# Kernel optimization log

Measured on AMD Instinct MI355X. Metric: run time of the kernel, lower is better.

Reference implementation:

```python
import jax, jax.numpy as jnp
import numpy as np

N_EMB = 1024
NUM_HEADS = 16
HEAD_DIM = N_EMB // NUM_HEADS
B, T = 4, 2048


def setup_inputs() -> dict:
    key = jax.random.key(0)
    k1, k2, k3, k4, k5 = jax.random.split(key, 5)
    s = 0.02
    return {
        "x": jax.random.normal(k1, (B, T, N_EMB), dtype=jnp.float32),
        "w_qkv": jax.random.normal(k2, (N_EMB, 3 * N_EMB), dtype=jnp.float32) * s,
        "b_qkv": jnp.zeros((3 * N_EMB,), dtype=jnp.float32),
        "w_proj": jax.random.normal(k3, (N_EMB, N_EMB), dtype=jnp.float32) * s,
        "b_proj": jnp.zeros((N_EMB,), dtype=jnp.float32),
    }


def reference(x, w_qkv, b_qkv, w_proj, b_proj):
    Bx, Tx, C = x.shape
    qkv = x @ w_qkv + b_qkv  # [B,T,3C]
    q, k, v = jnp.split(qkv, 3, axis=-1)
    # [B,H,T,D]
    def heads(t):
        return t.reshape(Bx, Tx, NUM_HEADS, HEAD_DIM).transpose(0, 2, 1, 3)
    q, k, v = heads(q), heads(k), heads(v)
    scale = 1.0 / np.sqrt(HEAD_DIM).astype(np.float32)
    att = jnp.einsum('bhqd,bhkd->bhqk', q, k) * scale
    causal = jnp.tril(jnp.ones((Tx, Tx), dtype=bool))
    att = jnp.where(causal[None, None], att, -jnp.inf)
    att = jax.nn.softmax(att, axis=-1)
    # dropout omitted (eval mode / deterministic reference)
    y = jnp.einsum('bhqk,bhkd->bhqd', att, v)
    y = y.transpose(0, 2, 1, 3).reshape(Bx, Tx, C)
    return y @ w_proj + b_proj
```

## Files before the change

### kernel.cpp

```cpp
#include <hip/hip_runtime.h>
#include <hip/hip_bf16.h>

typedef __attribute__((ext_vector_type(8))) short short8;
typedef __attribute__((ext_vector_type(4))) float f32x4;

static __device__ __forceinline__ unsigned short f2bf(float f) {
    unsigned int u = __builtin_bit_cast(unsigned int, f);
    u += 0x7fff + ((u >> 16) & 1);
    return (unsigned short)(u >> 16);
}

static __device__ __forceinline__ float bf2f(unsigned short u) {
    return __builtin_bit_cast(float, (unsigned int)u << 16);
}

static __device__ __forceinline__ void gl_lds16(const unsigned short* g, unsigned short* l) {
    __builtin_amdgcn_global_load_lds(
        (const __attribute__((address_space(1))) unsigned int*)g,
        (__attribute__((address_space(3))) unsigned int*)l, 16, 0, 0);
}

__global__ __launch_bounds__(256) void k_f32_to_bf16(
    const float* __restrict__ in, unsigned short* __restrict__ out, long n)
{
    long i = ((long)blockIdx.x * 256 + threadIdx.x) * 8;
    if (i >= n) return;
    const f32x4 a = *reinterpret_cast<const f32x4*>(in + i);
    const f32x4 b = *reinterpret_cast<const f32x4*>(in + i + 4);
    union { unsigned short u[8]; uint4 v; } o;
    o.u[0] = f2bf(a[0]); o.u[1] = f2bf(a[1]); o.u[2] = f2bf(a[2]); o.u[3] = f2bf(a[3]);
    o.u[4] = f2bf(b[0]); o.u[5] = f2bf(b[1]); o.u[6] = f2bf(b[2]); o.u[7] = f2bf(b[3]);
    *reinterpret_cast<uint4*>(out + i) = o.v;
}

__global__ __launch_bounds__(256) void k_transpose_w(
    const float* __restrict__ w, unsigned short* __restrict__ wt, int K, int N)
{
    __shared__ unsigned short tile[64][72];
    const int k0 = blockIdx.x * 64, n0 = blockIdx.y * 64;
    const int tid = threadIdx.x;
#pragma unroll
    for (int it = 0; it < 4; ++it) {
        int idx = it * 256 + tid;
        int kl = idx >> 4;
        int nl = (idx & 15) * 4;
        f32x4 v = *reinterpret_cast<const f32x4*>(w + (long)(k0 + kl) * N + n0 + nl);
        tile[kl][nl + 0] = f2bf(v[0]);
        tile[kl][nl + 1] = f2bf(v[1]);
        tile[kl][nl + 2] = f2bf(v[2]);
        tile[kl][nl + 3] = f2bf(v[3]);
    }
    __syncthreads();
#pragma unroll
    for (int it = 0; it < 2; ++it) {
        int idx = it * 256 + tid;
        int nl = idx >> 3;
        int c  = (idx & 7) * 8;
        union { unsigned short u[8]; uint4 v; } o;
#pragma unroll
        for (int j = 0; j < 8; ++j) o.u[j] = tile[c + j][nl];
        *reinterpret_cast<uint4*>(wt + (long)(n0 + nl) * K + k0 + c) = o.v;
    }
}

template <int OUTF32>
__global__ __launch_bounds__(256) void k_gemm_bt(
    const unsigned short* __restrict__ A,
    const unsigned short* __restrict__ Bt,
    const float* __restrict__ bias,
    void* __restrict__ Cv, int M, int N, int K)
{
    __shared__ unsigned short As[128][72];
    __shared__ unsigned short Bs[128][72];
    const int tid = threadIdx.x;
    const int m0 = blockIdx.x * 128;
    const int n0 = blockIdx.y * 128;
    const int w = tid >> 6, lane = tid & 63;
    const int wr = (w >> 1) * 64, wc = (w & 1) * 64;
    const int l4 = lane >> 4, l15 = lane & 15;

    f32x4 acc[4][4] = {};
    const int nk = K / 64;
    for (int kt = 0; kt < nk; ++kt) {
        const int k0 = kt * 64;
        __syncthreads();
#pragma unroll
        for (int it = 0; it < 4; ++it) {
            int idx = it * 256 + tid;
            int r = idx >> 3, c = (idx & 7) * 8;
            *reinterpret_cast<uint4*>(&As[r][c]) =
                *reinterpret_cast<const uint4*>(A + (long)(m0 + r) * K + k0 + c);
            *reinterpret_cast<uint4*>(&Bs[r][c]) =
                *reinterpret_cast<const uint4*>(Bt + (long)(n0 + r) * K + k0 + c);
        }
        __syncthreads();
#pragma unroll
        for (int kk = 0; kk < 2; ++kk) {
            short8 af[4], bf[4];
#pragma unroll
            for (int m = 0; m < 4; ++m)
                af[m] = *reinterpret_cast<const short8*>(&As[wr + m * 16 + l15][kk * 32 + l4 * 8]);
#pragma unroll
            for (int n = 0; n < 4; ++n)
                bf[n] = *reinterpret_cast<const short8*>(&Bs[wc + n * 16 + l15][kk * 32 + l4 * 8]);
#pragma unroll
            for (int m = 0; m < 4; ++m)
#pragma unroll
                for (int n = 0; n < 4; ++n)
                    acc[m][n] = __builtin_amdgcn_mfma_f32_16x16x32_bf16(af[m], bf[n], acc[m][n], 0, 0, 0);
        }
    }
#pragma unroll
    for (int n = 0; n < 4; ++n) {
        const int col = n0 + wc + n * 16 + l15;
        const float bv = bias[col];
#pragma unroll
        for (int m = 0; m < 4; ++m) {
            const int row = m0 + wr + m * 16 + l4 * 4;
#pragma unroll
            for (int i = 0; i < 4; ++i) {
                float v = acc[m][n][i] + bv;
                if (OUTF32)
                    reinterpret_cast<float*>(Cv)[(long)(row + i) * N + col] = v;
                else
                    reinterpret_cast<unsigned short*>(Cv)[(long)(row + i) * N + col] = f2bf(v);
            }
        }
    }
}

__global__ __launch_bounds__(256) void k_transpose_v(
    const unsigned short* __restrict__ qkv, unsigned short* __restrict__ vt, int T)
{
    __shared__ unsigned short tile[64][72];
    const int t0 = blockIdx.x * 64, bh = blockIdx.y;
    const int b = bh >> 4, h = bh & 15;
    const int tid = threadIdx.x;
#pragma unroll
    for (int it = 0; it < 2; ++it) {
        int idx = it * 256 + tid;
        int r = idx >> 3, c = (idx & 7) * 8;
        *reinterpret_cast<uint4*>(&tile[r][c]) =
            *reinterpret_cast<const uint4*>(qkv + (long)(b * T + t0 + r) * 3072 + 2048 + h * 64 + c);
    }
    __syncthreads();
#pragma unroll
    for (int it = 0; it < 2; ++it) {
        int idx = it * 256 + tid;
        int d = idx >> 3, c = (idx & 7) * 8;
        union { unsigned short u[8]; uint4 v; } o;
#pragma unroll
        for (int j = 0; j < 8; ++j) o.u[j] = tile[c + j][d];
        *reinterpret_cast<uint4*>(vt + ((long)bh * 64 + d) * T + t0 + c) = o.v;
    }
}

__global__ __launch_bounds__(256, 3) void k_attn(
    const unsigned short* __restrict__ qkv,
    const unsigned short* __restrict__ vt,
    unsigned short* __restrict__ y, int T)
{
    __shared__ __align__(16) unsigned short Kb[2][64][64];
    __shared__ __align__(16) unsigned short Vb[2][64][64];
    __shared__ unsigned short Ps[4][16][64];
    const int nQT = T >> 6;

    int n = blockIdx.x + gridDim.x * blockIdx.y;
    n = (n & 7) * ((gridDim.x * gridDim.y) >> 3) + (n >> 3);
    const int qa = n & 15;
    const int qb = nQT - 1 - qa;
    const int bh = n >> 4;
    const int b = bh >> 4, h = bh & 15;
    const int tid = threadIdx.x, w = tid >> 6, lane = tid & 63;
    const int l4 = lane >> 4, l15 = lane & 15;

    const float SC = 0.125f * 1.44269504f;

    const unsigned short* qpA = qkv + (long)(b * T + qa * 64 + w * 16 + l15) * 3072 + h * 64;
    const unsigned short* qpB = qkv + (long)(b * T + qb * 64 + w * 16 + l15) * 3072 + h * 64;
    short8 qfA[2], qfB[2];
    qfA[0] = *reinterpret_cast<const short8*>(qpA + l4 * 8);
    qfA[1] = *reinterpret_cast<const short8*>(qpA + 32 + l4 * 8);
    qfB[0] = *reinterpret_cast<const short8*>(qpB + l4 * 8);
    qfB[1] = *reinterpret_cast<const short8*>(qpB + 32 + l4 * 8);
#pragma unroll
    for (int kk = 0; kk < 2; ++kk)
#pragma unroll
        for (int j = 0; j < 8; ++j) {
            qfA[kk][j] = (short)f2bf(bf2f((unsigned short)qfA[kk][j]) * SC);
            qfB[kk][j] = (short)f2bf(bf2f((unsigned short)qfB[kk][j]) * SC);
        }

    short8 onesf;
#pragma unroll
    for (int j = 0; j < 8; ++j) onesf[j] = (short)0x3F80;

    const int lrow  = lane >> 3;
    const int lslot = (lane & 7) ^ lrow;
    const unsigned short* kg = qkv + (long)b * T * 3072 + 1024 + h * 64 + lslot * 8;
    const unsigned short* vg = vt + (long)bh * 64 * T + lslot * 8;

    auto stage = [&](int buf, int kt) {
#pragma unroll
        for (int i = 0; i < 2; ++i) {
            const int rb = (w * 2 + i) * 8;
            gl_lds16(kg + (long)(kt * 64 + rb + lrow) * 3072, &Kb[buf][rb][0]);
            gl_lds16(vg + (long)(rb + lrow) * T + kt * 64,    &Vb[buf][rb][0]);
        }
    };

    f32x4 oA[4] = {}, oB[4] = {};
    f32x4 lsA = {}, lsB = {};
    const int qrow = w * 16 + l4 * 4;
    int cur = 0;

    auto do_tile = [&](const short8 (&qf)[2], f32x4 (&o)[4], f32x4 &ls,
                       bool diag) {
        f32x4 s[4] = {};
        __builtin_amdgcn_s_setprio(1);
#pragma unroll
        for (int kk = 0; kk < 2; ++kk)
#pragma unroll
            for (int c = 0; c < 4; ++c) {
                const int r = c * 16 + l15;
                short8 kf = *reinterpret_cast<const short8*>(
                    &Kb[cur][r][(((kk * 4 + l4) ^ (r & 7)) * 8)]);
                s[c] = __builtin_amdgcn_mfma_f32_16x16x32_bf16(qf[kk], kf, s[c], 0, 0, 0);
            }
        __builtin_amdgcn_s_setprio(0);
#pragma unroll
        for (int c = 0; c < 4; ++c)
#pragma unroll
            for (int i = 0; i < 4; ++i) {
                float p = exp2f(s[c][i]);
                if (diag && (c * 16 + l15 > qrow + i)) p = 0.f;
                const int pr = l4 * 4 + i;
                Ps[w][pr][(c * 16 + l15) ^ ((pr & 7) << 3)] =
                    (unsigned short)(__builtin_bit_cast(unsigned int, p) >> 16);
            }
        __builtin_amdgcn_s_setprio(1);
#pragma unroll
        for (int kk = 0; kk < 2; ++kk) {
            short8 pf = *reinterpret_cast<const short8*>(
                &Ps[w][l15][(((kk * 4 + l4) ^ (l15 & 7)) * 8)]);
            ls = __builtin_amdgcn_mfma_f32_16x16x32_bf16(pf, onesf, ls, 0, 0, 0);
#pragma unroll
            for (int nn = 0; nn < 4; ++nn) {
                const int r = nn * 16 + l15;
                short8 vf = *reinterpret_cast<const short8*>(
                    &Vb[cur][r][(((kk * 4 + l4) ^ (r & 7)) * 8)]);
                o[nn] = __builtin_amdgcn_mfma_f32_16x16x32_bf16(pf, vf, o[nn], 0, 0, 0);
            }
        }
        __builtin_amdgcn_s_setprio(0);
    };

    stage(0, 0);
    __syncthreads();
    for (int kt = 0; kt <= qb; ++kt) {
        if (kt < qb) stage(cur ^ 1, kt + 1);
        do_tile(qfB, oB, lsB, kt == qb);
        if (kt <= qa) do_tile(qfA, oA, lsA, kt == qa);
        __syncthreads();
        cur ^= 1;
    }

#pragma unroll
    for (int i = 0; i < 4; ++i) {
        float invA = 1.f / lsA[i];
        float invB = 1.f / lsB[i];
        int qArow = qa * 64 + w * 16 + l4 * 4 + i;
        int qBrow = qb * 64 + w * 16 + l4 * 4 + i;
        unsigned short* ypA = y + (long)(b * T + qArow) * 1024 + h * 64;
        unsigned short* ypB = y + (long)(b * T + qBrow) * 1024 + h * 64;
#pragma unroll
        for (int nn = 0; nn < 4; ++nn) {
            ypA[nn * 16 + l15] = f2bf(oA[nn][i] * invA);
            ypB[nn * 16 + l15] = f2bf(oB[nn][i] * invB);
        }
    }
}

extern "C" void kernel_launch(void* const* d_in, const int* in_sizes, int n_in,
                              void* d_out, int out_size, void* d_ws, size_t ws_size,
                              hipStream_t stream) {
    const float* x      = (const float*)d_in[0];
    const float* w_qkv  = (const float*)d_in[1];
    const float* b_qkv  = (const float*)d_in[2];
    const float* w_proj = (const float*)d_in[3];
    const float* b_proj = (const float*)d_in[4];
    float* out = (float*)d_out;

    const int B = 4, T = 2048, C = 1024, H = 16;
    const long M = (long)B * T;

    char* ws = (char*)d_ws;
    unsigned short* xb  = (unsigned short*)ws; ws += M * C * 2;
    unsigned short* wqt = (unsigned short*)ws; ws += (long)3 * C * C * 2;
    unsigned short* wpt = (unsigned short*)ws; ws += (long)C * C * 2;
    unsigned short* qkv = (unsigned short*)ws; ws += M * 3 * C * 2;
    unsigned short* vt  = (unsigned short*)ws; ws += M * C * 2;
    unsigned short* y   = (unsigned short*)ws; ws += M * C * 2;

    k_f32_to_bf16<<<(int)((M * C / 8 + 255) / 256), 256, 0, stream>>>(x, xb, M * C);
    {
        dim3 g(C / 64, 3 * C / 64);
        k_transpose_w<<<g, 256, 0, stream>>>(w_qkv, wqt, C, 3 * C);
    }
    {
        dim3 g(C / 64, C / 64);
        k_transpose_w<<<g, 256, 0, stream>>>(w_proj, wpt, C, C);
    }
    {
        dim3 g(M / 128, 3 * C / 128);
        k_gemm_bt<0><<<g, 256, 0, stream>>>(xb, wqt, b_qkv, qkv, (int)M, 3 * C, C);
    }
    {
        dim3 g(T / 64, B * H);
        k_transpose_v<<<g, 256, 0, stream>>>(qkv, vt, T);
    }
    {
        dim3 g(T / 128, B * H);
        k_attn<<<g, 256, 0, stream>>>(qkv, vt, y, T);
    }
    {
        dim3 g(M / 128, C / 128);
        k_gemm_bt<1><<<g, 256, 0, stream>>>(y, wpt, b_proj, out, (int)M, C, C);
    }
}
```

Before: 190.2 us.

## Switch attention to 32x32x16 MFMA with transposed scores and register P exchange

Rewrites the attention inner loop to compute S^T with 32x32x16 bf16 MFMAs, so that each wave handles its 16 rows of both paired query tiles (A and B) together in one 32-column block. The probabilities are packed to bf16 and swapped between half-waves with shuffles instead of a round trip through the LDS Ps buffer, and the output is written as packed 8-byte stores. Dropping the Ps shared array and raising the launch-bounds occupancy target from 3 to 4 aims at more waves per CU. In exchange, the A-tile lanes do masked but still-executed work on key tiles beyond their causal limit, and register pressure is higher under the tighter launch bound.

```diff
diff --git a/kernel.cpp b/kernel.cpp
--- a/kernel.cpp
+++ b/kernel.cpp
@@ -3,6 +3,7 @@
 
 typedef __attribute__((ext_vector_type(8))) short short8;
 typedef __attribute__((ext_vector_type(4))) float f32x4;
+typedef __attribute__((ext_vector_type(16))) float f32x16;
 
 static __device__ __forceinline__ unsigned short f2bf(float f) {
     unsigned int u = __builtin_bit_cast(unsigned int, f);
@@ -12,6 +13,11 @@
 
 static __device__ __forceinline__ float bf2f(unsigned short u) {
     return __builtin_bit_cast(float, (unsigned int)u << 16);
+}
+
+static __device__ __forceinline__ unsigned int pkbf(float a, float b) {
+    return (__builtin_bit_cast(unsigned int, b) & 0xffff0000u) |
+           (__builtin_bit_cast(unsigned int, a) >> 16);
 }
 
 static __device__ __forceinline__ void gl_lds16(const unsigned short* g, unsigned short* l) {
@@ -155,14 +161,13 @@
     }
 }
 
-__global__ __launch_bounds__(256, 3) void k_attn(
+__global__ __launch_bounds__(256, 4) void k_attn(
     const unsigned short* __restrict__ qkv,
     const unsigned short* __restrict__ vt,
     unsigned short* __restrict__ y, int T)
 {
     __shared__ __align__(16) unsigned short Kb[2][64][64];
     __shared__ __align__(16) unsigned short Vb[2][64][64];
-    __shared__ unsigned short Ps[4][16][64];
     const int nQT = T >> 6;
 
     int n = blockIdx.x + gridDim.x * blockIdx.y;
@@ -170,26 +175,24 @@
     const int qa = n & 15;
     const int qb = nQT - 1 - qa;
     const int bh = n >> 4;
-    const int b = bh >> 4, h = bh & 15;
+    const int b = bh >> 4, hd = bh & 15;
     const int tid = threadIdx.x, w = tid >> 6, lane = tid & 63;
-    const int l4 = lane >> 4, l15 = lane & 15;
+    const int q31 = lane & 31, h = lane >> 5, h4 = h * 4;
+    const bool isA = q31 >= 16;
+    const int qloc = w * 16 + (q31 & 15);
+    const int q_global = (isA ? qa : qb) * 64 + qloc;
 
     const float SC = 0.125f * 1.44269504f;
 
-    const unsigned short* qpA = qkv + (long)(b * T + qa * 64 + w * 16 + l15) * 3072 + h * 64;
-    const unsigned short* qpB = qkv + (long)(b * T + qb * 64 + w * 16 + l15) * 3072 + h * 64;
-    short8 qfA[2], qfB[2];
-    qfA[0] = *reinterpret_cast<const short8*>(qpA + l4 * 8);
-    qfA[1] = *reinterpret_cast<const short8*>(qpA + 32 + l4 * 8);
-    qfB[0] = *reinterpret_cast<const short8*>(qpB + l4 * 8);
-    qfB[1] = *reinterpret_cast<const short8*>(qpB + 32 + l4 * 8);
-#pragma unroll
-    for (int kk = 0; kk < 2; ++kk)
-#pragma unroll
-        for (int j = 0; j < 8; ++j) {
-            qfA[kk][j] = (short)f2bf(bf2f((unsigned short)qfA[kk][j]) * SC);
-            qfB[kk][j] = (short)f2bf(bf2f((unsigned short)qfB[kk][j]) * SC);
-        }
+    const unsigned short* qp = qkv + (long)(b * T + q_global) * 3072 + hd * 64 + h * 8;
+    short8 qf[4];
+#pragma unroll
+    for (int s = 0; s < 4; ++s) {
+        qf[s] = *reinterpret_cast<const short8*>(qp + s * 16);
+#pragma unroll
+        for (int j = 0; j < 8; ++j)
+            qf[s][j] = (short)f2bf(bf2f((unsigned short)qf[s][j]) * SC);
+    }
 
     short8 onesf;
 #pragma unroll
@@ -197,7 +200,7 @@
 
     const int lrow  = lane >> 3;
     const int lslot = (lane & 7) ^ lrow;
-    const unsigned short* kg = qkv + (long)b * T * 3072 + 1024 + h * 64 + lslot * 8;
+    const unsigned short* kg = qkv + (long)b * T * 3072 + 1024 + hd * 64 + lslot * 8;
     const unsigned short* vg = vt + (long)bh * 64 * T + lslot * 8;
 
     auto stage = [&](int buf, int kt) {
@@ -209,76 +212,91 @@
         }
     };
 
-    f32x4 oA[4] = {}, oB[4] = {};
-    f32x4 lsA = {}, lsB = {};
-    const int qrow = w * 16 + l4 * 4;
+    f32x16 oT[2] = {};
+    f32x16 ls = {};
     int cur = 0;
-
-    auto do_tile = [&](const short8 (&qf)[2], f32x4 (&o)[4], f32x4 &ls,
-                       bool diag) {
-        f32x4 s[4] = {};
-        __builtin_amdgcn_s_setprio(1);
-#pragma unroll
-        for (int kk = 0; kk < 2; ++kk)
-#pragma unroll
-            for (int c = 0; c < 4; ++c) {
-                const int r = c * 16 + l15;
-                short8 kf = *reinterpret_cast<const short8*>(
-                    &Kb[cur][r][(((kk * 4 + l4) ^ (r & 7)) * 8)]);
-                s[c] = __builtin_amdgcn_mfma_f32_16x16x32_bf16(qf[kk], kf, s[c], 0, 0, 0);
-            }
-        __builtin_amdgcn_s_setprio(0);
-#pragma unroll
-        for (int c = 0; c < 4; ++c)
-#pragma unroll
-            for (int i = 0; i < 4; ++i) {
-                float p = exp2f(s[c][i]);
-                if (diag && (c * 16 + l15 > qrow + i)) p = 0.f;
-                const int pr = l4 * 4 + i;
-                Ps[w][pr][(c * 16 + l15) ^ ((pr & 7) << 3)] =
-                    (unsigned short)(__builtin_bit_cast(unsigned int, p) >> 16);
-            }
-        __builtin_amdgcn_s_setprio(1);
-#pragma unroll
-        for (int kk = 0; kk < 2; ++kk) {
-            short8 pf = *reinterpret_cast<const short8*>(
-                &Ps[w][l15][(((kk * 4 + l4) ^ (l15 & 7)) * 8)]);
-            ls = __builtin_amdgcn_mfma_f32_16x16x32_bf16(pf, onesf, ls, 0, 0, 0);
-#pragma unroll
-            for (int nn = 0; nn < 4; ++nn) {
-                const int r = nn * 16 + l15;
-                short8 vf = *reinterpret_cast<const short8*>(
-                    &Vb[cur][r][(((kk * 4 + l4) ^ (r & 7)) * 8)]);
-                o[nn] = __builtin_amdgcn_mfma_f32_16x16x32_bf16(pf, vf, o[nn], 0, 0, 0);
-            }
-        }
-        __builtin_amdgcn_s_setprio(0);
-    };
 
     stage(0, 0);
     __syncthreads();
     for (int kt = 0; kt <= qb; ++kt) {
         if (kt < qb) stage(cur ^ 1, kt + 1);
-        do_tile(qfB, oB, lsB, kt == qb);
-        if (kt <= qa) do_tile(qfA, oA, lsA, kt == qa);
+
+        int qlim;
+        if (!isA) qlim = (kt == qb) ? qloc : 63;
+        else      qlim = (kt < qa) ? 63 : ((kt == qa) ? qloc : -1);
+
+#pragma unroll
+        for (int c2 = 0; c2 < 2; ++c2) {
+            f32x16 s = {};
+            __builtin_amdgcn_s_setprio(1);
+#pragma unroll
+            for (int s4 = 0; s4 < 4; ++s4) {
+                const int r = c2 * 32 + q31;
+                short8 kf = *reinterpret_cast<const short8*>(
+                    &Kb[cur][r][(((s4 * 2 + h) ^ (r & 7)) * 8)]);
+                s = __builtin_amdgcn_mfma_f32_32x32x16_bf16(kf, qf[s4], s, 0, 0, 0);
+            }
+            __builtin_amdgcn_s_setprio(0);
+
+            float p[16];
+#pragma unroll
+            for (int r = 0; r < 16; ++r) {
+                const int kl = c2 * 32 + (r & 3) + 8 * (r >> 2) + h4;
+                p[r] = (kl <= qlim) ? exp2f(s[r]) : 0.f;
+            }
+            unsigned int A0 = pkbf(p[0], p[1]),  B0 = pkbf(p[2], p[3]);
+            unsigned int C0 = pkbf(p[4], p[5]),  D0 = pkbf(p[6], p[7]);
+            unsigned int E0 = pkbf(p[8], p[9]),  F0 = pkbf(p[10], p[11]);
+            unsigned int G0 = pkbf(p[12], p[13]), H0 = pkbf(p[14], p[15]);
+            unsigned int xA = __shfl_xor((int)A0, 32), xB = __shfl_xor((int)B0, 32);
+            unsigned int xC = __shfl_xor((int)C0, 32), xD = __shfl_xor((int)D0, 32);
+            unsigned int xE = __shfl_xor((int)E0, 32), xF = __shfl_xor((int)F0, 32);
+            unsigned int xG = __shfl_xor((int)G0, 32), xH = __shfl_xor((int)H0, 32);
+
+#pragma unroll
+            for (int ss = 0; ss < 2; ++ss) {
+                union { unsigned int u[4]; short8 v; } pf;
+                if (ss == 0) {
+                    pf.u[0] = h ? xC : A0;  pf.u[1] = h ? xD : B0;
+                    pf.u[2] = h ? C0 : xA;  pf.u[3] = h ? D0 : xB;
+                } else {
+                    pf.u[0] = h ? xG : E0;  pf.u[1] = h ? xH : F0;
+                    pf.u[2] = h ? G0 : xE;  pf.u[3] = h ? H0 : xF;
+                }
+                const int ks = c2 * 2 + ss;
+                __builtin_amdgcn_s_setprio(1);
+                ls = __builtin_amdgcn_mfma_f32_32x32x16_bf16(onesf, pf.v, ls, 0, 0, 0);
+#pragma unroll
+                for (int db = 0; db < 2; ++db) {
+                    const int r = db * 32 + q31;
+                    short8 vf = *reinterpret_cast<const short8*>(
+                        &Vb[cur][r][(((ks * 2 + h) ^ (r & 7)) * 8)]);
+                    oT[db] = __builtin_amdgcn_mfma_f32_32x32x16_bf16(vf, pf.v, oT[db], 0, 0, 0);
+                }
+                __builtin_amdgcn_s_setprio(0);
+            }
+        }
         __syncthreads();
         cur ^= 1;
     }
 
-#pragma unroll
-    for (int i = 0; i < 4; ++i) {
-        float invA = 1.f / lsA[i];
-        float invB = 1.f / lsB[i];
-        int qArow = qa * 64 + w * 16 + l4 * 4 + i;
-        int qBrow = qb * 64 + w * 16 + l4 * 4 + i;
-        unsigned short* ypA = y + (long)(b * T + qArow) * 1024 + h * 64;
-        unsigned short* ypB = y + (long)(b * T + qBrow) * 1024 + h * 64;
-#pragma unroll
-        for (int nn = 0; nn < 4; ++nn) {
-            ypA[nn * 16 + l15] = f2bf(oA[nn][i] * invA);
-            ypB[nn * 16 + l15] = f2bf(oB[nn][i] * invB);
-        }
-    }
+    const float inv = 1.f / ls[0];
+    unsigned short* yp = y + (long)(b * T + q_global) * 1024 + hd * 64;
+#pragma unroll
+    for (int db = 0; db < 2; ++db)
+#pragma unroll
+        for (int g = 0; g < 4; ++g) {
+            const int d0 = db * 32 + 8 * g + h4;
+            unsigned int u0 = (pkbf(0.f, oT[db][4 * g + 1] * inv) & 0xffff0000u) |
+                              ((unsigned int)f2bf(oT[db][4 * g + 0] * inv));
+            unsigned int u1 = (pkbf(0.f, oT[db][4 * g + 3] * inv) & 0xffff0000u) |
+                              ((unsigned int)f2bf(oT[db][4 * g + 2] * inv));
+            u0 = ((unsigned int)f2bf(oT[db][4 * g + 1] * inv) << 16) |
+                 (unsigned int)f2bf(oT[db][4 * g + 0] * inv);
+            u1 = ((unsigned int)f2bf(oT[db][4 * g + 3] * inv) << 16) |
+                 (unsigned int)f2bf(oT[db][4 * g + 2] * inv);
+            *reinterpret_cast<uint2*>(yp + d0) = make_uint2(u0, u1);
+        }
 }
 
 extern "C" void kernel_launch(void* const* d_in, const int* in_sizes, int n_in,
```

Measured after the change: 235.0 us. +23.5%, slower.
